# Optimization experiments

Hardware: AMD Instinct MI355X
Metric: run time of the kernel (lower is better)

Reference implementation:

```python
import jax, jax.numpy as jnp
import numpy as np

N = 100000        # num_nodes
E_HALF = 800000   # directed edges; full symmetric edge list has 2*E_HALF
D = 64            # feature dim (hard-coded Linear(64,64) in source)
STEP = 1.0        # step_size


def setup_inputs() -> dict:
    key = jax.random.key(0)
    k1, k2, k3, k4, k5, k6 = jax.random.split(key, 6)
    src = jax.random.randint(k1, (E_HALF,), 0, N)
    dst = jax.random.randint(k2, (E_HALF,), 0, N)
    # symmetric edge list: edge e in [0,E_HALF) has its reverse at e+E_HALF
    edge_index = jnp.stack([jnp.concatenate([src, dst]),
                            jnp.concatenate([dst, src])])  # (2, 2*E_HALF)
    left_idx = jnp.arange(2 * E_HALF)
    right_idx = jnp.concatenate([jnp.arange(E_HALF, 2 * E_HALF),
                                 jnp.arange(0, E_HALF)])
    x = jax.random.normal(k3, (N, D), dtype=jnp.float32)
    W_sheaf = jax.random.normal(k4, (1, 2 * D), dtype=jnp.float32) * 0.08  # sheaf_learner (128->1, no bias)
    W_lin = jax.random.normal(k5, (D, D), dtype=jnp.float32) * 0.125       # linear 64->64
    b_lin = jax.random.normal(k6, (D,), dtype=jnp.float32) * 0.01
    return {"x": x, "W_sheaf": W_sheaf, "W_lin": W_lin, "b_lin": b_lin,
            "edge_index": edge_index, "left_idx": left_idx, "right_idx": right_idx}


def reference(x, W_sheaf, W_lin, b_lin, edge_index, left_idx, right_idx):
    row, col = edge_index[0], edge_index[1]
    # predict_restriction_maps: gather endpoints, concat, linear, tanh -> (E,1)
    x_row = x[row]
    x_col = x[col]
    maps = jnp.tanh(jnp.concatenate([x_row, x_col], axis=1) @ W_sheaf.T)  # (E,1)
    # build_laplacian
    left_maps = maps[left_idx]
    right_maps = maps[right_idx]
    non_diag_maps = -left_maps * right_maps                                # (E,1)
    diag_maps = jax.ops.segment_sum(maps ** 2, row, num_segments=N)       # (N,1)
    d_sqrt_inv = jax.lax.rsqrt(diag_maps + 1.0)                            # (N,1)
    norm_maps = d_sqrt_inv[row] * non_diag_maps * d_sqrt_inv[col]          # (E,1)
    diag = d_sqrt_inv * diag_maps * d_sqrt_inv                             # (N,1)
    # y = linear(x); sparse Laplacian @ y = diag part + scatter-add of edge part
    y = x @ W_lin.T + b_lin                                                # (N,D)
    Ly = diag * y + jax.ops.segment_sum(norm_maps * y[col], row, num_segments=N)
    return x - STEP * Ly
```

## Files before the change

kernel.cpp:

```cpp
#include <hip/hip_runtime.h>
#include <hip/hip_fp16.h>


#define NBLK_BIN 256

__global__ __launch_bounds__(256) void k_pre_hist(
    const float* __restrict__ x,
    const float* __restrict__ Wsheaf,
    const float* __restrict__ Wlin,
    const float* __restrict__ blin,
    float2* __restrict__ s12,
    __half* __restrict__ yz,
    const int* __restrict__ row, const int* __restrict__ col,
    unsigned* __restrict__ table,
    int N, int Eh, int NB, int NPRE)
{
    __shared__ float4 xt[64 * 16];
    int tid = threadIdx.x;

    if (blockIdx.x >= NPRE) {
        unsigned* h = (unsigned*)xt;
        int hb = blockIdx.x - NPRE;
        for (int i = tid; i < NB; i += 256) h[i] = 0;
        __syncthreads();
        int chunk = (Eh + NBLK_BIN - 1) / NBLK_BIN;
        int lo = hb * chunk, hi = min(lo + chunk, Eh);
        for (int i = lo + tid; i < hi; i += 256) {
            atomicAdd(&h[(unsigned)row[i] >> 8], 1u);
            atomicAdd(&h[(unsigned)col[i] >> 8], 1u);
        }
        __syncthreads();
        for (int i = tid; i < NB; i += 256) table[(size_t)hb * NB + i] = h[i];
        return;
    }

    int lane = tid & 63;
    int wave = tid >> 6;
    int n0   = blockIdx.x * 64;

    float wreg[64];
    {
        const float4* Wv = (const float4*)(Wlin + lane * 64);
        #pragma unroll
        for (int q = 0; q < 16; ++q) {
            float4 w4 = Wv[q];
            wreg[4 * q + 0] = w4.x; wreg[4 * q + 1] = w4.y;
            wreg[4 * q + 2] = w4.z; wreg[4 * q + 3] = w4.w;
        }
    }
    float bl  = blin[lane];
    float ws1 = Wsheaf[lane];
    float ws2 = Wsheaf[64 + lane];

    int nvalid = min(64, N - n0);
    const float4* xg = (const float4*)(x + (size_t)n0 * 64);
    for (int i = tid; i < nvalid * 16; i += 256) xt[i] = xg[i];
    __syncthreads();

    int ni_end = min(wave * 16 + 16, nvalid);
    for (int ni = wave * 16; ni < ni_end; ++ni) {
        float xv = ((const float*)xt)[ni * 64 + lane];
        float a = xv * ws1, b = xv * ws2;
        #pragma unroll
        for (int m = 32; m; m >>= 1) {
            a += __shfl_xor(a, m);
            b += __shfl_xor(b, m);
        }
        if (lane == 0) s12[n0 + ni] = make_float2(a, b);

        float acc = bl;
        #pragma unroll
        for (int q = 0; q < 16; ++q) {
            float4 xq = xt[ni * 16 + q];
            acc += xq.x * wreg[4 * q + 0] + xq.y * wreg[4 * q + 1]
                 + xq.z * wreg[4 * q + 2] + xq.w * wreg[4 * q + 3];
        }
        yz[(size_t)(n0 + ni) * 64 + lane] = __float2half(acc);
    }
}

__global__ __launch_bounds__(256) void k_colscan(
    unsigned* __restrict__ table, unsigned* __restrict__ colsum, int NB)
{
    __shared__ unsigned sm[256];
    int j = blockIdx.x, t = threadIdx.x;
    unsigned v = table[(size_t)t * NB + j];
    sm[t] = v;
    __syncthreads();
    for (int off = 1; off < 256; off <<= 1) {
        unsigned u = (t >= off) ? sm[t - off] : 0;
        __syncthreads();
        if (t >= off) sm[t] += u;
        __syncthreads();
    }
    table[(size_t)t * NB + j] = sm[t] - v;
    if (t == 255) colsum[j] = sm[255];
}

__global__ __launch_bounds__(512) void k_binplace(
    const float2* __restrict__ s12,
    const int* __restrict__ row, const int* __restrict__ col,
    const unsigned* __restrict__ table, const unsigned* __restrict__ colsum,
    uint2* __restrict__ binned, int Eh, int NB)
{
    __shared__ unsigned csum[512];
    __shared__ unsigned destbase[512];
    __shared__ unsigned cur[512];
    int t = threadIdx.x;

    unsigned v = (t < NB) ? colsum[t] : 0;
    csum[t] = v;
    __syncthreads();
    for (int off = 1; off < 512; off <<= 1) {
        unsigned u = (t >= off) ? csum[t - off] : 0;
        __syncthreads();
        csum[t] += u;
        __syncthreads();
    }
    if (t < NB) {
        destbase[t] = (csum[t] - v) + table[(size_t)blockIdx.x * NB + t];
        cur[t] = 0;
    }
    __syncthreads();

    int chunk = (Eh + NBLK_BIN - 1) / NBLK_BIN;
    int lo = blockIdx.x * chunk, hi = min(lo + chunk, Eh);
    for (int i = lo + t; i < hi; i += 512) {
        int r = row[i], c = col[i];
        float2 sr = s12[r], sc2 = s12[c];
        float mf = tanhf(sr.x + sc2.y);
        float mr = tanhf(sc2.x + sr.y);
        float pr = mf * mr;

        __half2 h1 = __halves2half2(__float2half_rn(mf * mf), __float2half_rn(pr));
        unsigned u1 = *reinterpret_cast<unsigned*>(&h1);
        unsigned bk_r = (unsigned)r >> 8;
        unsigned d1 = destbase[bk_r] + atomicAdd(&cur[bk_r], 1u);
        binned[d1] = make_uint2(((unsigned)(r & 255) << 17) | (unsigned)c, u1);

        __half2 h2 = __halves2half2(__float2half_rn(mr * mr), __float2half_rn(pr));
        unsigned u2 = *reinterpret_cast<unsigned*>(&h2);
        unsigned bk_c = (unsigned)c >> 8;
        unsigned d2 = destbase[bk_c] + atomicAdd(&cur[bk_c], 1u);
        binned[d2] = make_uint2(((unsigned)(c & 255) << 17) | (unsigned)r, u2);
    }
}

__global__ __launch_bounds__(256) void k_bucket(
    const uint2* __restrict__ binned,
    const unsigned* __restrict__ colsum,
    int* __restrict__ base, float* __restrict__ dinv,
    int2* __restrict__ sc,
    __half* __restrict__ yz,
    int N, int NB)
{
    __shared__ unsigned cnt[256];
    __shared__ float dsum[256];
    __shared__ unsigned pref[256];
    __shared__ unsigned cur[256];
    __shared__ float sdinv[256];
    __shared__ unsigned red[256];

    int b = blockIdx.x, t = threadIdx.x;
    int row0 = b << 8;

    unsigned part = 0;
    for (int j = t; j < b; j += 256) part += colsum[j];
    red[t] = part;
    cnt[t] = 0;
    dsum[t] = 0.0f;
    __syncthreads();
    for (int m = 128; m; m >>= 1) {
        if (t < m) red[t] += red[t + m];
        __syncthreads();
    }
    int lo = (int)red[0];
    int hi = lo + (int)colsum[b];

    for (int i = lo + t; i < hi; i += 256) {
        uint2 v = binned[i];
        unsigned rl = v.x >> 17;
        atomicAdd(&cnt[rl], 1u);
        __half2 h = *reinterpret_cast<__half2*>(&v.y);
        atomicAdd(&dsum[rl], __low2float(h));
    }
    __syncthreads();

    unsigned myc = cnt[t];
    pref[t] = myc;
    __syncthreads();
    for (int off = 1; off < 256; off <<= 1) {
        unsigned u = (t >= off) ? pref[t - off] : 0;
        __syncthreads();
        if (t >= off) pref[t] += u;
        __syncthreads();
    }
    unsigned excl = pref[t] - myc;
    float dv = rsqrtf(dsum[t] + 1.0f);
    sdinv[t] = dv;
    int rown = row0 + t;
    if (rown < N) {
        base[rown] = lo + (int)excl;
        dinv[rown] = dv;
    }
    if (b == (int)gridDim.x - 1 && t == 0) base[N] = hi;
    cur[t] = excl;
    __syncthreads();

    for (int i = lo + t; i < hi; i += 256) {
        uint2 v = binned[i];
        unsigned rl = v.x >> 17;
        unsigned other = v.x & 0x1FFFFu;
        unsigned slot = (unsigned)lo + atomicAdd(&cur[rl], 1u);
        __half2 h = *reinterpret_cast<__half2*>(&v.y);
        sc[slot] = make_int2((int)other, __float_as_int(__high2float(h)));
    }

    for (int i = t; i < 256 * 64; i += 256) {
        int rl = i >> 6;
        int rn = row0 + rl;
        if (rn < N) {
            size_t idx = (size_t)rn * 64 + (i & 63);
            yz[idx] = __float2half(sdinv[rl] * __half2float(yz[idx]));
        }
    }
}

__global__ __launch_bounds__(256) void k_node_gather(
    const float* __restrict__ x,
    const __half* __restrict__ zh,
    const float* __restrict__ dinv,
    const int* __restrict__ base,
    const int2* __restrict__ sc,
    float* __restrict__ out,
    int N)
{
    __shared__ int2 stage[4][64];
    int lane = threadIdx.x & 63;
    int wave = threadIdx.x >> 6;
    int n = blockIdx.x * 4 + wave;
    if (n >= N) return;

    int j0 = base[n], end = base[n + 1];
    float acc = 0.0f;
    for (int blk = j0; blk < end; blk += 64) {
        int m = min(64, end - blk);
        if (lane < m) stage[wave][lane] = sc[blk + lane];
        #pragma unroll 4
        for (int j = 0; j < m; ++j) {
            int2 r = stage[wave][j];
            acc += __int_as_float(r.y) * __half2float(zh[(size_t)r.x * 64 + lane]);
        }
    }
    float dv = dinv[n];
    int idx = n * 64 + lane;
    float zv = __half2float(zh[idx]);
    out[idx] = x[idx] - (1.0f / dv - dv) * zv + dv * acc;
}

extern "C" void kernel_launch(void* const* d_in, const int* in_sizes, int n_in,
                              void* d_out, int out_size, void* d_ws, size_t ws_size,
                              hipStream_t stream) {
    const float* x      = (const float*)d_in[0];
    const float* Wsheaf = (const float*)d_in[1];
    const float* Wlin   = (const float*)d_in[2];
    const float* blin   = (const float*)d_in[3];
    const int*   ei     = (const int*)d_in[4];
    float* out = (float*)d_out;

    int N  = in_sizes[0] / 64;
    int E  = in_sizes[4] / 2;
    int Eh = E >> 1;
    int NB = (N + 255) >> 8;
    int NPRE = (N + 63) / 64;
    const int* row = ei;
    const int* col = ei + E;

    char* ws = (char*)d_ws;
    float2*   s12    = (float2*)ws;             ws += (size_t)N * 8;
    uint2*    binned = (uint2*)ws;              ws += (size_t)E * 8;
    int2*     sc     = (int2*)ws;               ws += (size_t)E * 8;
    unsigned* table  = (unsigned*)ws;           ws += (size_t)NBLK_BIN * NB * 4;
    unsigned* colsum = (unsigned*)ws;           ws += (size_t)NB * 4;
    int*      base   = (int*)ws;                ws += (size_t)(N + 1) * 4;
    float*    dinv   = (float*)ws;              ws += (size_t)N * 4;
    __half*   yz     = (__half*)ws;             ws += (size_t)N * 64 * 2;

    k_pre_hist <<<NPRE + NBLK_BIN, 256, 0, stream>>>(x, Wsheaf, Wlin, blin, s12, yz,
                                                     row, col, table, N, Eh, NB, NPRE);
    k_colscan  <<<NB, 256, 0, stream>>>(table, colsum, NB);
    k_binplace <<<NBLK_BIN, 512, 0, stream>>>(s12, row, col, table, colsum, binned, Eh, NB);
    k_bucket   <<<NB, 256, 0, stream>>>(binned, colsum, base, dinv, sc, yz, N, NB);
    k_node_gather<<<(N + 3) / 4, 256, 0, stream>>>(x, yz, dinv, base, sc, out, N);
}
```

Baseline: 256.8 us.

## Drop per-row CSR sort; accumulate bucketed edges into LDS tiles in gather

Removes the second counting-sort pass, which built per-row CSR (base/sc). The final gather now processes each 256-row bucket in a 512-thread block that reads binned records directly and accumulates into a 64KB shared-memory tile with LDS atomics. binplace now stages records per block in LDS before scattering them, so global writes land in contiguous runs. The trade is LDS atomic contention, lower occupancy from the large shared tiles, and only NB (~391) blocks in the gather.

```diff
diff --git a/kernel.cpp b/kernel.cpp
--- a/kernel.cpp
+++ b/kernel.cpp
@@ -3,6 +3,8 @@
 
 
 #define NBLK_BIN 256
+#define CHUNK_CAP 4096
+#define STAGE_CAP 8192
 
 __global__ __launch_bounds__(256) void k_pre_hist(
     const float* __restrict__ x,
@@ -97,7 +99,7 @@
     if (t == 255) colsum[j] = sm[255];
 }
 
-__global__ __launch_bounds__(512) void k_binplace(
+__global__ __launch_bounds__(512, 1) void k_binplace(
     const float2* __restrict__ s12,
     const int* __restrict__ row, const int* __restrict__ col,
     const unsigned* __restrict__ table, const unsigned* __restrict__ colsum,
@@ -105,7 +107,13 @@
 {
     __shared__ unsigned csum[512];
     __shared__ unsigned destbase[512];
+    __shared__ unsigned h[512];
+    __shared__ unsigned locex[512];
     __shared__ unsigned cur[512];
+    __shared__ uint2    stg[STAGE_CAP];
+    __shared__ unsigned gaddr[STAGE_CAP];
+    __shared__ __half2  pm[CHUNK_CAP];
+
     int t = threadIdx.x;
 
     unsigned v = (t < NB) ? colsum[t] : 0;
@@ -117,49 +125,92 @@
         csum[t] += u;
         __syncthreads();
     }
-    if (t < NB) {
-        destbase[t] = (csum[t] - v) + table[(size_t)blockIdx.x * NB + t];
-        cur[t] = 0;
-    }
+    if (t < NB) destbase[t] = (csum[t] - v) + table[(size_t)blockIdx.x * NB + t];
+    h[t] = 0;
+    cur[t] = 0;
     __syncthreads();
 
     int chunk = (Eh + NBLK_BIN - 1) / NBLK_BIN;
     int lo = blockIdx.x * chunk, hi = min(lo + chunk, Eh);
-    for (int i = lo + t; i < hi; i += 512) {
-        int r = row[i], c = col[i];
-        float2 sr = s12[r], sc2 = s12[c];
-        float mf = tanhf(sr.x + sc2.y);
-        float mr = tanhf(sc2.x + sr.y);
-        float pr = mf * mr;
-
-        __half2 h1 = __halves2half2(__float2half_rn(mf * mf), __float2half_rn(pr));
-        unsigned u1 = *reinterpret_cast<unsigned*>(&h1);
-        unsigned bk_r = (unsigned)r >> 8;
-        unsigned d1 = destbase[bk_r] + atomicAdd(&cur[bk_r], 1u);
-        binned[d1] = make_uint2(((unsigned)(r & 255) << 17) | (unsigned)c, u1);
-
-        __half2 h2 = __halves2half2(__float2half_rn(mr * mr), __float2half_rn(pr));
-        unsigned u2 = *reinterpret_cast<unsigned*>(&h2);
-        unsigned bk_c = (unsigned)c >> 8;
-        unsigned d2 = destbase[bk_c] + atomicAdd(&cur[bk_c], 1u);
-        binned[d2] = make_uint2(((unsigned)(c & 255) << 17) | (unsigned)r, u2);
-    }
-}
-
-__global__ __launch_bounds__(256) void k_bucket(
+
+    if (chunk <= CHUNK_CAP) {
+        for (int i = lo + t; i < hi; i += 512) {
+            int r = row[i], c = col[i];
+            float2 sr = s12[r], sc2 = s12[c];
+            float mf = tanhf(sr.x + sc2.y);
+            float mr = tanhf(sc2.x + sr.y);
+            pm[i - lo] = __halves2half2(__float2half_rn(mf), __float2half_rn(mr));
+            atomicAdd(&h[(unsigned)r >> 8], 1u);
+            atomicAdd(&h[(unsigned)c >> 8], 1u);
+        }
+        __syncthreads();
+        unsigned hv = h[t];
+        csum[t] = hv;
+        __syncthreads();
+        for (int off = 1; off < 512; off <<= 1) {
+            unsigned u = (t >= off) ? csum[t - off] : 0;
+            __syncthreads();
+            csum[t] += u;
+            __syncthreads();
+        }
+        locex[t] = csum[t] - hv;
+        __syncthreads();
+        for (int i = lo + t; i < hi; i += 512) {
+            int r = row[i], c = col[i];
+            __half2 m = pm[i - lo];
+            float mf = __low2float(m), mr = __high2float(m);
+            float pr = mf * mr;
+
+            unsigned bk_r = (unsigned)r >> 8;
+            unsigned pos1 = atomicAdd(&cur[bk_r], 1u);
+            unsigned s1i  = locex[bk_r] + pos1;
+            __half2 h1 = __halves2half2(__float2half_rn(mf * mf), __float2half_rn(pr));
+            stg[s1i]   = make_uint2(((unsigned)(r & 255) << 17) | (unsigned)c,
+                                    *reinterpret_cast<unsigned*>(&h1));
+            gaddr[s1i] = destbase[bk_r] + pos1;
+
+            unsigned bk_c = (unsigned)c >> 8;
+            unsigned pos2 = atomicAdd(&cur[bk_c], 1u);
+            unsigned s2i  = locex[bk_c] + pos2;
+            __half2 h2 = __halves2half2(__float2half_rn(mr * mr), __float2half_rn(pr));
+            stg[s2i]   = make_uint2(((unsigned)(c & 255) << 17) | (unsigned)r,
+                                    *reinterpret_cast<unsigned*>(&h2));
+            gaddr[s2i] = destbase[bk_c] + pos2;
+        }
+        __syncthreads();
+        int total = (hi > lo) ? 2 * (hi - lo) : 0;
+        for (int i = t; i < total; i += 512) binned[gaddr[i]] = stg[i];
+    } else {
+        for (int i = lo + t; i < hi; i += 512) {
+            int r = row[i], c = col[i];
+            float2 sr = s12[r], sc2 = s12[c];
+            float mf = tanhf(sr.x + sc2.y);
+            float mr = tanhf(sc2.x + sr.y);
+            float pr = mf * mr;
+            __half2 h1 = __halves2half2(__float2half_rn(mf * mf), __float2half_rn(pr));
+            unsigned bk_r = (unsigned)r >> 8;
+            unsigned d1 = destbase[bk_r] + atomicAdd(&cur[bk_r], 1u);
+            binned[d1] = make_uint2(((unsigned)(r & 255) << 17) | (unsigned)c,
+                                    *reinterpret_cast<unsigned*>(&h1));
+            __half2 h2 = __halves2half2(__float2half_rn(mr * mr), __float2half_rn(pr));
+            unsigned bk_c = (unsigned)c >> 8;
+            unsigned d2 = destbase[bk_c] + atomicAdd(&cur[bk_c], 1u);
+            binned[d2] = make_uint2(((unsigned)(c & 255) << 17) | (unsigned)r,
+                                    *reinterpret_cast<unsigned*>(&h2));
+        }
+    }
+}
+
+__global__ __launch_bounds__(256) void k_diag(
     const uint2* __restrict__ binned,
     const unsigned* __restrict__ colsum,
-    int* __restrict__ base, float* __restrict__ dinv,
-    int2* __restrict__ sc,
+    float* __restrict__ dinv,
     __half* __restrict__ yz,
     int N, int NB)
 {
-    __shared__ unsigned cnt[256];
     __shared__ float dsum[256];
-    __shared__ unsigned pref[256];
-    __shared__ unsigned cur[256];
-    __shared__ float sdinv[256];
     __shared__ unsigned red[256];
+    __shared__ float sdv[256];
 
     int b = blockIdx.x, t = threadIdx.x;
     int row0 = b << 8;
@@ -167,7 +218,6 @@
     unsigned part = 0;
     for (int j = t; j < b; j += 256) part += colsum[j];
     red[t] = part;
-    cnt[t] = 0;
     dsum[t] = 0.0f;
     __syncthreads();
     for (int m = 128; m; m >>= 1) {
@@ -179,83 +229,98 @@
 
     for (int i = lo + t; i < hi; i += 256) {
         uint2 v = binned[i];
-        unsigned rl = v.x >> 17;
-        atomicAdd(&cnt[rl], 1u);
         __half2 h = *reinterpret_cast<__half2*>(&v.y);
-        atomicAdd(&dsum[rl], __low2float(h));
-    }
-    __syncthreads();
-
-    unsigned myc = cnt[t];
-    pref[t] = myc;
-    __syncthreads();
-    for (int off = 1; off < 256; off <<= 1) {
-        unsigned u = (t >= off) ? pref[t - off] : 0;
-        __syncthreads();
-        if (t >= off) pref[t] += u;
-        __syncthreads();
-    }
-    unsigned excl = pref[t] - myc;
+        atomicAdd(&dsum[v.x >> 17], __low2float(h));
+    }
+    __syncthreads();
+
     float dv = rsqrtf(dsum[t] + 1.0f);
-    sdinv[t] = dv;
-    int rown = row0 + t;
-    if (rown < N) {
-        base[rown] = lo + (int)excl;
-        dinv[rown] = dv;
-    }
-    if (b == (int)gridDim.x - 1 && t == 0) base[N] = hi;
-    cur[t] = excl;
-    __syncthreads();
-
-    for (int i = lo + t; i < hi; i += 256) {
-        uint2 v = binned[i];
-        unsigned rl = v.x >> 17;
-        unsigned other = v.x & 0x1FFFFu;
-        unsigned slot = (unsigned)lo + atomicAdd(&cur[rl], 1u);
-        __half2 h = *reinterpret_cast<__half2*>(&v.y);
-        sc[slot] = make_int2((int)other, __float_as_int(__high2float(h)));
-    }
-
-    for (int i = t; i < 256 * 64; i += 256) {
-        int rl = i >> 6;
-        int rn = row0 + rl;
-        if (rn < N) {
-            size_t idx = (size_t)rn * 64 + (i & 63);
-            yz[idx] = __float2half(sdinv[rl] * __half2float(yz[idx]));
-        }
-    }
-}
-
-__global__ __launch_bounds__(256) void k_node_gather(
+    sdv[t] = dv;
+    int rn = row0 + t;
+    if (rn < N) dinv[rn] = dv;
+    __syncthreads();
+
+    __half2* yz2 = (__half2*)yz;
+    for (int i = t; i < 256 * 32; i += 256) {
+        int rl = i >> 5;
+        int rn2 = row0 + rl;
+        if (rn2 < N) {
+            size_t idx = (size_t)rn2 * 32 + (i & 31);
+            __half2 v = yz2[idx];
+            float s = sdv[rl];
+            yz2[idx] = __floats2half2_rn(s * __low2float(v), s * __high2float(v));
+        }
+    }
+}
+
+__global__ __launch_bounds__(512, 2) void k_gather(
     const float* __restrict__ x,
     const __half* __restrict__ zh,
     const float* __restrict__ dinv,
-    const int* __restrict__ base,
-    const int2* __restrict__ sc,
+    const uint2* __restrict__ binned,
+    const unsigned* __restrict__ colsum,
     float* __restrict__ out,
-    int N)
-{
-    __shared__ int2 stage[4][64];
-    int lane = threadIdx.x & 63;
-    int wave = threadIdx.x >> 6;
-    int n = blockIdx.x * 4 + wave;
-    if (n >= N) return;
-
-    int j0 = base[n], end = base[n + 1];
-    float acc = 0.0f;
-    for (int blk = j0; blk < end; blk += 64) {
-        int m = min(64, end - blk);
-        if (lane < m) stage[wave][lane] = sc[blk + lane];
-        #pragma unroll 4
-        for (int j = 0; j < m; ++j) {
-            int2 r = stage[wave][j];
-            acc += __int_as_float(r.y) * __half2float(zh[(size_t)r.x * 64 + lane]);
-        }
-    }
-    float dv = dinv[n];
-    int idx = n * 64 + lane;
-    float zv = __half2float(zh[idx]);
-    out[idx] = x[idx] - (1.0f / dv - dv) * zv + dv * acc;
+    int N, int NB)
+{
+    __shared__ float acc[256 * 64];
+    __shared__ unsigned red[512];
+
+    int t = threadIdx.x, b = blockIdx.x;
+    int row0 = b << 8;
+    int lane = t & 63, wave = t >> 6;
+
+    unsigned part = 0;
+    for (int j = t; j < b; j += 512) part += colsum[j];
+    red[t] = part;
+    __syncthreads();
+    for (int m = 256; m; m >>= 1) {
+        if (t < m) red[t] += red[t + m];
+        __syncthreads();
+    }
+    int lo = (int)red[0];
+    int hi = lo + (int)colsum[b];
+
+    for (int i = t; i < 256 * 64; i += 512) acc[i] = 0.0f;
+    __syncthreads();
+
+    for (int b64 = lo + wave * 64; b64 < hi; b64 += 8 * 64) {
+        int m = min(64, hi - b64);
+        uint2 rec = (lane < m) ? binned[b64 + lane] : make_uint2(0u, 0u);
+        if (m == 64) {
+            #pragma unroll 4
+            for (int j = 0; j < 64; ++j) {
+                unsigned kx = __shfl(rec.x, j);
+                unsigned ky = __shfl(rec.y, j);
+                unsigned rl = kx >> 17, other = kx & 0x1FFFFu;
+                __half2 h = *reinterpret_cast<__half2*>(&ky);
+                float pr = __high2float(h);
+                float zv = __half2float(zh[(size_t)other * 64 + lane]);
+                atomicAdd(&acc[(rl << 6) | lane], pr * zv);
+            }
+        } else {
+            for (int j = 0; j < m; ++j) {
+                unsigned kx = __shfl(rec.x, j);
+                unsigned ky = __shfl(rec.y, j);
+                unsigned rl = kx >> 17, other = kx & 0x1FFFFu;
+                __half2 h = *reinterpret_cast<__half2*>(&ky);
+                float pr = __high2float(h);
+                float zv = __half2float(zh[(size_t)other * 64 + lane]);
+                atomicAdd(&acc[(rl << 6) | lane], pr * zv);
+            }
+        }
+    }
+    __syncthreads();
+
+    for (int i = t; i < 256 * 64; i += 512) {
+        int rl = i >> 6, ln = i & 63;
+        int rn = row0 + rl;
+        if (rn < N) {
+            float dv = dinv[rn];
+            size_t idx = (size_t)rn * 64 + ln;
+            float zv = __half2float(zh[idx]);
+            out[idx] = x[idx] - (1.0f / dv - dv) * zv + dv * acc[i];
+        }
+    }
 }
 
 extern "C" void kernel_launch(void* const* d_in, const int* in_sizes, int n_in,
@@ -279,10 +344,8 @@
     char* ws = (char*)d_ws;
     float2*   s12    = (float2*)ws;             ws += (size_t)N * 8;
     uint2*    binned = (uint2*)ws;              ws += (size_t)E * 8;
-    int2*     sc     = (int2*)ws;               ws += (size_t)E * 8;
     unsigned* table  = (unsigned*)ws;           ws += (size_t)NBLK_BIN * NB * 4;
     unsigned* colsum = (unsigned*)ws;           ws += (size_t)NB * 4;
-    int*      base   = (int*)ws;                ws += (size_t)(N + 1) * 4;
     float*    dinv   = (float*)ws;              ws += (size_t)N * 4;
     __half*   yz     = (__half*)ws;             ws += (size_t)N * 64 * 2;
 
@@ -290,6 +353,6 @@
                                                      row, col, table, N, Eh, NB, NPRE);
     k_colscan  <<<NB, 256, 0, stream>>>(table, colsum, NB);
     k_binplace <<<NBLK_BIN, 512, 0, stream>>>(s12, row, col, table, colsum, binned, Eh, NB);
-    k_bucket   <<<NB, 256, 0, stream>>>(binned, colsum, base, dinv, sc, yz, N, NB);
-    k_node_gather<<<(N + 3) / 4, 256, 0, stream>>>(x, yz, dinv, base, sc, out, N);
-}
+    k_diag     <<<NB, 256, 0, stream>>>(binned, colsum, dinv, yz, N, NB);
+    k_gather   <<<NB, 512, 0, stream>>>(x, yz, dinv, binned, colsum, out, N, NB);
+}
```

Result: slower. 916.4 us (+256.8%).

## Stage binned edge records in LDS for coalesced bucket writes; vectorize yz scaling

Applied to the files above, without the earlier changes.

k_binplace now makes two passes over its edge chunk. The first computes the tanh maps, keeps them in LDS and builds a per-block bucket histogram. The second writes records into a locally sorted LDS staging buffer and then copies them to global memory, so consecutive threads write consecutive bucket slots instead of scattering each record separately. This is meant to cut the cost of uncoalesced global writes, but it uses a large amount of LDS (about 112 KB), which limits the kernel to one block per CU and adds extra syncs. The yz scaling loop in k_bucket is also switched to half2 loads and stores.

```diff
diff --git a/kernel.cpp b/kernel.cpp
--- a/kernel.cpp
+++ b/kernel.cpp
@@ -3,6 +3,8 @@
 
 
 #define NBLK_BIN 256
+#define CHUNK_CAP 4096
+#define STAGE_CAP 8192
 
 __global__ __launch_bounds__(256) void k_pre_hist(
     const float* __restrict__ x,
@@ -97,7 +99,7 @@
     if (t == 255) colsum[j] = sm[255];
 }
 
-__global__ __launch_bounds__(512) void k_binplace(
+__global__ __launch_bounds__(512, 1) void k_binplace(
     const float2* __restrict__ s12,
     const int* __restrict__ row, const int* __restrict__ col,
     const unsigned* __restrict__ table, const unsigned* __restrict__ colsum,
@@ -105,7 +107,13 @@
 {
     __shared__ unsigned csum[512];
     __shared__ unsigned destbase[512];
+    __shared__ unsigned h[512];
+    __shared__ unsigned locex[512];
     __shared__ unsigned cur[512];
+    __shared__ uint2    stg[STAGE_CAP];
+    __shared__ unsigned gaddr[STAGE_CAP];
+    __shared__ __half2  pm[CHUNK_CAP];
+
     int t = threadIdx.x;
 
     unsigned v = (t < NB) ? colsum[t] : 0;
@@ -117,32 +125,79 @@
         csum[t] += u;
         __syncthreads();
     }
-    if (t < NB) {
-        destbase[t] = (csum[t] - v) + table[(size_t)blockIdx.x * NB + t];
-        cur[t] = 0;
-    }
+    if (t < NB) destbase[t] = (csum[t] - v) + table[(size_t)blockIdx.x * NB + t];
+    h[t] = 0;
+    cur[t] = 0;
     __syncthreads();
 
     int chunk = (Eh + NBLK_BIN - 1) / NBLK_BIN;
     int lo = blockIdx.x * chunk, hi = min(lo + chunk, Eh);
-    for (int i = lo + t; i < hi; i += 512) {
-        int r = row[i], c = col[i];
-        float2 sr = s12[r], sc2 = s12[c];
-        float mf = tanhf(sr.x + sc2.y);
-        float mr = tanhf(sc2.x + sr.y);
-        float pr = mf * mr;
-
-        __half2 h1 = __halves2half2(__float2half_rn(mf * mf), __float2half_rn(pr));
-        unsigned u1 = *reinterpret_cast<unsigned*>(&h1);
-        unsigned bk_r = (unsigned)r >> 8;
-        unsigned d1 = destbase[bk_r] + atomicAdd(&cur[bk_r], 1u);
-        binned[d1] = make_uint2(((unsigned)(r & 255) << 17) | (unsigned)c, u1);
-
-        __half2 h2 = __halves2half2(__float2half_rn(mr * mr), __float2half_rn(pr));
-        unsigned u2 = *reinterpret_cast<unsigned*>(&h2);
-        unsigned bk_c = (unsigned)c >> 8;
-        unsigned d2 = destbase[bk_c] + atomicAdd(&cur[bk_c], 1u);
-        binned[d2] = make_uint2(((unsigned)(c & 255) << 17) | (unsigned)r, u2);
+
+    if (chunk <= CHUNK_CAP) {
+        for (int i = lo + t; i < hi; i += 512) {
+            int r = row[i], c = col[i];
+            float2 sr = s12[r], sc2 = s12[c];
+            float mf = tanhf(sr.x + sc2.y);
+            float mr = tanhf(sc2.x + sr.y);
+            pm[i - lo] = __halves2half2(__float2half_rn(mf), __float2half_rn(mr));
+            atomicAdd(&h[(unsigned)r >> 8], 1u);
+            atomicAdd(&h[(unsigned)c >> 8], 1u);
+        }
+        __syncthreads();
+        unsigned hv = h[t];
+        csum[t] = hv;
+        __syncthreads();
+        for (int off = 1; off < 512; off <<= 1) {
+            unsigned u = (t >= off) ? csum[t - off] : 0;
+            __syncthreads();
+            csum[t] += u;
+            __syncthreads();
+        }
+        locex[t] = csum[t] - hv;
+        __syncthreads();
+        for (int i = lo + t; i < hi; i += 512) {
+            int r = row[i], c = col[i];
+            __half2 m = pm[i - lo];
+            float mf = __low2float(m), mr = __high2float(m);
+            float pr = mf * mr;
+
+            unsigned bk_r = (unsigned)r >> 8;
+            unsigned pos1 = atomicAdd(&cur[bk_r], 1u);
+            unsigned s1i  = locex[bk_r] + pos1;
+            __half2 h1 = __halves2half2(__float2half_rn(mf * mf), __float2half_rn(pr));
+            stg[s1i]   = make_uint2(((unsigned)(r & 255) << 17) | (unsigned)c,
+                                    *reinterpret_cast<unsigned*>(&h1));
+            gaddr[s1i] = destbase[bk_r] + pos1;
+
+            unsigned bk_c = (unsigned)c >> 8;
+            unsigned pos2 = atomicAdd(&cur[bk_c], 1u);
+            unsigned s2i  = locex[bk_c] + pos2;
+            __half2 h2 = __halves2half2(__float2half_rn(mr * mr), __float2half_rn(pr));
+            stg[s2i]   = make_uint2(((unsigned)(c & 255) << 17) | (unsigned)r,
+                                    *reinterpret_cast<unsigned*>(&h2));
+            gaddr[s2i] = destbase[bk_c] + pos2;
+        }
+        __syncthreads();
+        int total = (hi > lo) ? 2 * (hi - lo) : 0;
+        for (int i = t; i < total; i += 512) binned[gaddr[i]] = stg[i];
+    } else {
+        for (int i = lo + t; i < hi; i += 512) {
+            int r = row[i], c = col[i];
+            float2 sr = s12[r], sc2 = s12[c];
+            float mf = tanhf(sr.x + sc2.y);
+            float mr = tanhf(sc2.x + sr.y);
+            float pr = mf * mr;
+            __half2 h1 = __halves2half2(__float2half_rn(mf * mf), __float2half_rn(pr));
+            unsigned bk_r = (unsigned)r >> 8;
+            unsigned d1 = destbase[bk_r] + atomicAdd(&cur[bk_r], 1u);
+            binned[d1] = make_uint2(((unsigned)(r & 255) << 17) | (unsigned)c,
+                                    *reinterpret_cast<unsigned*>(&h1));
+            __half2 h2 = __halves2half2(__float2half_rn(mr * mr), __float2half_rn(pr));
+            unsigned bk_c = (unsigned)c >> 8;
+            unsigned d2 = destbase[bk_c] + atomicAdd(&cur[bk_c], 1u);
+            binned[d2] = make_uint2(((unsigned)(c & 255) << 17) | (unsigned)r,
+                                    *reinterpret_cast<unsigned*>(&h2));
+        }
     }
 }
 
@@ -216,12 +271,15 @@
         sc[slot] = make_int2((int)other, __float_as_int(__high2float(h)));
     }
 
-    for (int i = t; i < 256 * 64; i += 256) {
-        int rl = i >> 6;
+    __half2* yz2 = (__half2*)yz;
+    for (int i = t; i < 256 * 32; i += 256) {
+        int rl = i >> 5;
         int rn = row0 + rl;
         if (rn < N) {
-            size_t idx = (size_t)rn * 64 + (i & 63);
-            yz[idx] = __float2half(sdinv[rl] * __half2float(yz[idx]));
+            size_t idx = (size_t)rn * 32 + (i & 31);
+            __half2 v = yz2[idx];
+            float s = sdinv[rl];
+            yz2[idx] = __floats2half2_rn(s * __low2float(v), s * __high2float(v));
         }
     }
 }
```

Result: faster. 246.7 us (-3.9%).
